# Optimization experiments

Hardware: AMD Instinct MI355X
Metric: run time of the kernel (lower is better)

The kernel has to match this reference:

```python
import jax, jax.numpy as jnp
import numpy as np

B, S, D, K = 4, 2048, 1024, 8

def setup_inputs() -> dict:
    key = jax.random.key(0)
    k1, k2, k3 = jax.random.split(key, 3)
    hidden_states = jax.random.normal(k1, (B, S, D), dtype=jnp.float32)
    # scaled so scores ~ O(1) and exp() does not overflow
    W_phi = jax.random.normal(k2, (D, D), dtype=jnp.float32) * 0.005
    W_psi = jax.random.normal(k3, (D, D), dtype=jnp.float32) * 0.005
    return {"hidden_states": hidden_states, "W_phi": W_phi, "W_psi": W_psi, "k": K}

def reference(hidden_states, W_phi, W_psi, k):
    b, s, d = hidden_states.shape
    k = min(k, s)
    # nn.Linear(bias=False): y = x @ W.T
    phi_h = hidden_states @ W_phi.T            # [b,s,d]
    psi_h = hidden_states @ W_psi.T            # [b,s,d]
    scores = jnp.einsum('bsd,btd->bst', phi_h, psi_h)  # [b,s,s]
    affinity = jnp.exp(scores)
    topk_values, topk_indices = jax.lax.top_k(affinity, k)   # [b,s,k]
    norm_sum = topk_values.sum(axis=-1, keepdims=True) + 1e-8
    normalized_weights = topk_values / norm_sum
    batch_offset = (jnp.arange(b) * s)[:, None, None]        # [b,1,1]
    src_local = jnp.arange(s)[None, :, None]                 # [1,s,1]
    src_global = jnp.broadcast_to(batch_offset + src_local, (b, s, k))
    dst_global = batch_offset + topk_indices
    mask = (topk_indices != src_local).reshape(-1)           # drop self-loops
    # eager boolean compaction (data-dependent size, like the torch module)
    src_final = src_global.reshape(-1)[mask]
    dst_final = dst_global.reshape(-1)[mask]
    weights_final = normalized_weights.reshape(-1)[mask]
    if src_final.size == 0:
        all_nodes = jnp.arange(b * s)
        return jnp.stack([all_nodes, all_nodes], axis=0), jnp.ones(b * s, dtype=jnp.float32)
    edge_index = jnp.stack([src_final, dst_final], axis=0)
    return edge_index, weights_final
```

## Files before the change

kernel.cpp:

```cpp
#include <hip/hip_runtime.h>
#include <cmath>

#define SEQ 2048
#define DDIM 1024
#define NROWS 8192
#define KSEL 8
#define NCAND 12
#define IMAXC 0x7fffffff

typedef __attribute__((ext_vector_type(8))) short bf16x8;
typedef __attribute__((ext_vector_type(4))) float f32x4;
typedef __attribute__((ext_vector_type(4))) double f64x4;

__device__ __forceinline__ unsigned short f2bf(float f) {
  unsigned u = __builtin_bit_cast(unsigned, f);
  u = (u + 0x7fffu + ((u >> 16) & 1u)) >> 16;
  return (unsigned short)u;
}
__device__ __forceinline__ float bf2f(unsigned short h) {
  unsigned u = ((unsigned)h) << 16;
  return __builtin_bit_cast(float, u);
}
__device__ __forceinline__ unsigned pkbf(float a, float b) {
  unsigned r;
  asm("v_cvt_pk_bf16_f32 %0, %1, %2" : "=v"(r) : "v"(a), "v"(b));
  return r;
}
__device__ __forceinline__ void dmap(int sel, int lg, int lr, int rg,
                                     int& ri, int& ci) {
  switch (sel) {
    case 0:  ri = (lg << 2) + rg; ci = lr; break;
    case 1:  ri = lg + (rg << 2); ci = lr; break;
    case 2:  ri = lr; ci = (lg << 2) + rg; break;
    default: ri = lr; ci = lg + (rg << 2); break;
  }
}

__global__ void kprobe(int* __restrict__ sel) {
  const int lane = threadIdx.x;
  const int lr = lane & 15, lg = lane >> 4;
  const double a = (double)(4 * lr + lg + 1);
  const double b = (double)(9 * lr + 5 * lg + 2);
  f64x4 d = (f64x4){0.0, 0.0, 0.0, 0.0};
  d = __builtin_amdgcn_mfma_f64_16x16x4f64(a, b, d, 0, 0, 0);
  int my = 4;
  for (int s = 3; s >= 0; --s) {
    bool ok = true;
    for (int rg = 0; rg < 4; ++rg) {
      int ri, ci;
      dmap(s, lg, lr, rg, ri, ci);
      double e = 0.0;
      for (int k = 0; k < 4; ++k)
        e += (double)(4 * ri + k + 1) * (double)(9 * ci + 5 * k + 2);
      ok = ok && (d[rg] == e);
    }
    if (__all(ok)) my = s;
  }
  if (lane == 0) sel[0] = my;
}

#define K0_STAGE(bi)                                        \
  do {                                                      \
    *reinterpret_cast<float4*>(&As[bi][kr][c4]) = pa0;      \
    *reinterpret_cast<float4*>(&As[bi][kr][c4 + 32]) = pa1; \
    *reinterpret_cast<float4*>(&Bs[bi][kr][c4]) = pb0;      \
    *reinterpret_cast<float4*>(&Bs[bi][kr][c4 + 32]) = pb1; \
  } while (0)

__global__ __launch_bounds__(256, 2)
void k0_mfma(const float* __restrict__ A, const float* __restrict__ B,
             float* __restrict__ C, const int* __restrict__ selp) {
  const int sel = selp[0];
  if (sel >= 4) return;
  __shared__ float As[2][32][72];
  __shared__ float Bs[2][32][72];
  const int tid = threadIdx.x;
  const int lane = tid & 63, w = tid >> 6;
  const int wr = w >> 1, wc = w & 1;
  const int lr = lane & 15, lg = lane >> 4;
  const int brow = blockIdx.y << 6, bcol = blockIdx.x << 6;
  const int kr = tid >> 3, c4 = (tid & 7) << 2;

  f64x4 acc[2][2];
#pragma unroll
  for (int mi = 0; mi < 2; ++mi)
#pragma unroll
    for (int nj = 0; nj < 2; ++nj)
      acc[mi][nj] = (f64x4){0.0, 0.0, 0.0, 0.0};

  const float* Ap = &A[(size_t)kr * DDIM + brow + c4];
  const float* Bp = &B[(size_t)kr * DDIM + bcol + c4];
  float4 pa0 = *reinterpret_cast<const float4*>(Ap);
  float4 pa1 = *reinterpret_cast<const float4*>(Ap + 32);
  float4 pb0 = *reinterpret_cast<const float4*>(Bp);
  float4 pb1 = *reinterpret_cast<const float4*>(Bp + 32);
  K0_STAGE(0);
  {
    const size_t nk = (size_t)32 * DDIM;
    pa0 = *reinterpret_cast<const float4*>(Ap + nk);
    pa1 = *reinterpret_cast<const float4*>(Ap + nk + 32);
    pb0 = *reinterpret_cast<const float4*>(Bp + nk);
    pb1 = *reinterpret_cast<const float4*>(Bp + nk + 32);
  }

  for (int t = 0; t < 32; ++t) {
    __syncthreads();
    const int cur = t & 1;
    if (t < 31) {
      K0_STAGE(cur ^ 1);
      if (t < 30) {
        const size_t nk = (size_t)(t + 2) * 32 * DDIM;
        pa0 = *reinterpret_cast<const float4*>(Ap + nk);
        pa1 = *reinterpret_cast<const float4*>(Ap + nk + 32);
        pb0 = *reinterpret_cast<const float4*>(Bp + nk);
        pb1 = *reinterpret_cast<const float4*>(Bp + nk + 32);
      }
    }
    __builtin_amdgcn_s_setprio(1);
#pragma unroll
    for (int kp = 0; kp < 8; ++kp) {
      const int ka = (kp << 2) + lg;
      double a[2], b[2];
#pragma unroll
      for (int mi = 0; mi < 2; ++mi)
        a[mi] = (double)As[cur][ka][(wr << 5) + (mi << 4) + lr];
#pragma unroll
      for (int nj = 0; nj < 2; ++nj)
        b[nj] = (double)Bs[cur][ka][(wc << 5) + (nj << 4) + lr];
#pragma unroll
      for (int mi = 0; mi < 2; ++mi)
#pragma unroll
        for (int nj = 0; nj < 2; ++nj)
          acc[mi][nj] = __builtin_amdgcn_mfma_f64_16x16x4f64(
              a[mi], b[nj], acc[mi][nj], 0, 0, 0);
    }
    __builtin_amdgcn_s_setprio(0);
  }
#pragma unroll
  for (int mi = 0; mi < 2; ++mi)
#pragma unroll
    for (int nj = 0; nj < 2; ++nj)
#pragma unroll
      for (int rg = 0; rg < 4; ++rg) {
        int ri, ci;
        dmap(sel, lg, lr, rg, ri, ci);
        C[(size_t)(brow + (wr << 5) + (mi << 4) + ri) * DDIM +
          bcol + (wc << 5) + (nj << 4) + ci] = (float)acc[mi][nj][rg];
      }
}

__global__ __launch_bounds__(256)
void k0_repair(const float* __restrict__ A, const float* __restrict__ B,
               float* __restrict__ C, const int* __restrict__ selp) {
  if (selp[0] < 4) return;
  __shared__ __align__(16) float As[32][68];
  __shared__ __align__(16) float Bs[32][68];
  const int tid = threadIdx.x;
  const int tx = tid & 15, ty = tid >> 4;
  const int brow = blockIdx.y << 6;
  const int bcol = blockIdx.x << 6;
  double acc[4][4] = {};
  for (int k0 = 0; k0 < DDIM; k0 += 32) {
#pragma unroll
    for (int i = 0; i < 2; ++i) {
      const int f = tid + (i << 8);
      const int r = f >> 4;
      const int c4 = (f & 15) << 2;
      *reinterpret_cast<float4*>(&As[r][c4]) =
          *reinterpret_cast<const float4*>(&A[(size_t)(k0 + r) * DDIM + brow + c4]);
      *reinterpret_cast<float4*>(&Bs[r][c4]) =
          *reinterpret_cast<const float4*>(&B[(size_t)(k0 + r) * DDIM + bcol + c4]);
    }
    __syncthreads();
#pragma unroll
    for (int kk = 0; kk < 32; ++kk) {
      const float4 a = *reinterpret_cast<const float4*>(&As[kk][ty << 2]);
      const float4 b = *reinterpret_cast<const float4*>(&Bs[kk][tx << 2]);
      const double ad[4] = {a.x, a.y, a.z, a.w};
      const double bd[4] = {b.x, b.y, b.z, b.w};
#pragma unroll
      for (int i = 0; i < 4; ++i)
#pragma unroll
        for (int j = 0; j < 4; ++j)
          acc[i][j] = fma(ad[i], bd[j], acc[i][j]);
    }
    __syncthreads();
  }
#pragma unroll
  for (int i = 0; i < 4; ++i) {
    float4 v = make_float4((float)acc[i][0], (float)acc[i][1],
                           (float)acc[i][2], (float)acc[i][3]);
    *reinterpret_cast<float4*>(
        &C[(size_t)(brow + (ty << 2) + i) * DDIM + bcol + (tx << 2)]) = v;
  }
}

#define K1_STAGE(bi)                                              \
  do {                                                            \
    As[bi][akh + 0][ar] = pa0.x; As[bi][akh + 1][ar] = pa0.y;     \
    As[bi][akh + 2][ar] = pa0.z; As[bi][akh + 3][ar] = pa0.w;     \
    As[bi][akh + 4][ar] = pa1.x; As[bi][akh + 5][ar] = pa1.y;     \
    As[bi][akh + 6][ar] = pa1.z; As[bi][akh + 7][ar] = pa1.w;     \
    *reinterpret_cast<float4*>(&Bs[bi][bk][bc4]) = pb0;           \
    *reinterpret_cast<float4*>(&Bs[bi][bk][bc4 + 64]) = pb1;      \
  } while (0)

__global__ __launch_bounds__(256, 2)
void k1_mfma(const float* __restrict__ A, const float* __restrict__ B,
             float* __restrict__ C, const int* __restrict__ selp) {
  const int sel = selp[0];
  if (sel >= 4) return;
  __shared__ float As[2][16][144];
  __shared__ float Bs[2][16][144];
  const int tid = threadIdx.x;
  const int lin = blockIdx.y * 8 + blockIdx.x;
  const int nlin = (lin & 7) * 64 + (lin >> 3);
  const int brow = (nlin >> 3) << 7;
  const int bcol = (nlin & 7) << 7;
  const int lane = tid & 63, w = tid >> 6;
  const int wr = w >> 1, wc = w & 1;
  const int lr = lane & 15, lg = lane >> 4;
  const int ar = tid >> 1, akh = (tid & 1) << 3;
  const int bk = tid >> 4, bc4 = (tid & 15) << 2;

  f64x4 acc[4][4];
#pragma unroll
  for (int mi = 0; mi < 4; ++mi)
#pragma unroll
    for (int nj = 0; nj < 4; ++nj)
      acc[mi][nj] = (f64x4){0.0, 0.0, 0.0, 0.0};

  const float* Ap = &A[(size_t)(brow + ar) * DDIM + akh];
  const float* Bp = &B[(size_t)bk * DDIM + bcol + bc4];

  float4 pa0 = *reinterpret_cast<const float4*>(Ap);
  float4 pa1 = *reinterpret_cast<const float4*>(Ap + 4);
  float4 pb0 = *reinterpret_cast<const float4*>(Bp);
  float4 pb1 = *reinterpret_cast<const float4*>(Bp + 64);
  K1_STAGE(0);
  pa0 = *reinterpret_cast<const float4*>(Ap + 16);
  pa1 = *reinterpret_cast<const float4*>(Ap + 20);
  pb0 = *reinterpret_cast<const float4*>(Bp + (size_t)16 * DDIM);
  pb1 = *reinterpret_cast<const float4*>(Bp + (size_t)16 * DDIM + 64);

  for (int t = 0; t < 64; ++t) {
    __syncthreads();
    const int cur = t & 1;
    if (t < 63) {
      K1_STAGE(cur ^ 1);
      if (t < 62) {
        const size_t ko = (size_t)(t + 2) << 4;
        pa0 = *reinterpret_cast<const float4*>(Ap + ko);
        pa1 = *reinterpret_cast<const float4*>(Ap + ko + 4);
        pb0 = *reinterpret_cast<const float4*>(Bp + ko * DDIM);
        pb1 = *reinterpret_cast<const float4*>(Bp + ko * DDIM + 64);
      }
    }
    __builtin_amdgcn_s_setprio(1);
#pragma unroll
    for (int kp = 0; kp < 4; ++kp) {
      const int ka = (kp << 2) + lg;
      double a[4], b[4];
#pragma unroll
      for (int mi = 0; mi < 4; ++mi)
        a[mi] = (double)As[cur][ka][(wr << 6) + (mi << 4) + lr];
#pragma unroll
      for (int nj = 0; nj < 4; ++nj)
        b[nj] = (double)Bs[cur][ka][(wc << 6) + (nj << 4) + lr];
#pragma unroll
      for (int mi = 0; mi < 4; ++mi)
#pragma unroll
        for (int nj = 0; nj < 4; ++nj)
          acc[mi][nj] = __builtin_amdgcn_mfma_f64_16x16x4f64(
              a[mi], b[nj], acc[mi][nj], 0, 0, 0);
    }
    __builtin_amdgcn_s_setprio(0);
  }
#pragma unroll
  for (int mi = 0; mi < 4; ++mi)
#pragma unroll
    for (int nj = 0; nj < 4; ++nj)
#pragma unroll
      for (int rg = 0; rg < 4; ++rg) {
        int ri, ci;
        dmap(sel, lg, lr, rg, ri, ci);
        C[(size_t)(brow + (wr << 6) + (mi << 4) + ri) * DDIM +
          bcol + (wc << 6) + (nj << 4) + ci] = (float)acc[mi][nj][rg];
      }
}

__global__ __launch_bounds__(256, 2)
void k1_repair(const float* __restrict__ A, const float* __restrict__ B,
               float* __restrict__ C, const int* __restrict__ selp) {
  if (selp[0] < 4) return;
  __shared__ double As[128][17];
  __shared__ double Bs[16][130];
  const int tid = threadIdx.x;
  const int lin = blockIdx.y * 8 + blockIdx.x;
  const int nlin = (lin & 7) * 64 + (lin >> 3);
  const int brow = (nlin >> 3) << 7;
  const int bcol = (nlin & 7) << 7;
  const int tx = tid & 15, ty = tid >> 4;
  const int ar = tid >> 1, aks = (tid & 1) << 3;
  const int bk = tid >> 4, btx = tid & 15;

  double acc[8][8];
#pragma unroll
  for (int i = 0; i < 8; ++i)
#pragma unroll
    for (int j = 0; j < 8; ++j) acc[i][j] = 0.0;

  const float* Aptr = &A[(size_t)(brow + ar) * DDIM + aks];
  const float* Bptr = &B[(size_t)bk * DDIM + bcol + (btx << 1)];

  float4 pa0, pa1;
  float2 pb[4];
  pa0 = *reinterpret_cast<const float4*>(Aptr);
  pa1 = *reinterpret_cast<const float4*>(Aptr + 4);
#pragma unroll
  for (int w = 0; w < 4; ++w)
    pb[w] = *reinterpret_cast<const float2*>(Bptr + (w << 5));

  for (int k0 = 0; k0 < DDIM; k0 += 16) {
    __syncthreads();
    As[ar][aks + 0] = (double)pa0.x; As[ar][aks + 1] = (double)pa0.y;
    As[ar][aks + 2] = (double)pa0.z; As[ar][aks + 3] = (double)pa0.w;
    As[ar][aks + 4] = (double)pa1.x; As[ar][aks + 5] = (double)pa1.y;
    As[ar][aks + 6] = (double)pa1.z; As[ar][aks + 7] = (double)pa1.w;
#pragma unroll
    for (int w = 0; w < 4; ++w) {
      Bs[bk][(btx << 1) + (w << 5) + 0] = (double)pb[w].x;
      Bs[bk][(btx << 1) + (w << 5) + 1] = (double)pb[w].y;
    }
    __syncthreads();
    if (k0 + 16 < DDIM) {
      pa0 = *reinterpret_cast<const float4*>(Aptr + k0 + 16);
      pa1 = *reinterpret_cast<const float4*>(Aptr + k0 + 20);
#pragma unroll
      for (int w = 0; w < 4; ++w)
        pb[w] = *reinterpret_cast<const float2*>(
            Bptr + (size_t)(k0 + 16) * DDIM + (w << 5));
    }
#pragma unroll 8
    for (int kk = 0; kk < 16; ++kk) {
      double a[8];
      double2 b[4];
#pragma unroll
      for (int i = 0; i < 8; ++i) a[i] = As[(ty << 3) + i][kk];
#pragma unroll
      for (int jj = 0; jj < 4; ++jj)
        b[jj] = *reinterpret_cast<const double2*>(&Bs[kk][(tx << 1) + (jj << 5)]);
#pragma unroll
      for (int i = 0; i < 8; ++i) {
#pragma unroll
        for (int jj = 0; jj < 4; ++jj) {
          acc[i][(jj << 1) + 0] = fma(a[i], b[jj].x, acc[i][(jj << 1) + 0]);
          acc[i][(jj << 1) + 1] = fma(a[i], b[jj].y, acc[i][(jj << 1) + 1]);
        }
      }
    }
  }
#pragma unroll
  for (int i = 0; i < 8; ++i) {
    float* crow = &C[(size_t)(brow + (ty << 3) + i) * DDIM + bcol + (tx << 1)];
#pragma unroll
    for (int jj = 0; jj < 4; ++jj) {
      float2 v = make_float2((float)acc[i][(jj << 1)],
                             (float)acc[i][(jj << 1) + 1]);
      *reinterpret_cast<float2*>(crow + (jj << 5)) = v;
    }
  }
}

#define K2_LOAD(koff)                                                         \
  do {                                                                        \
    _Pragma("unroll")                                                         \
    for (int q = 0; q < 4; ++q) {                                             \
      const int c = (q << 9) + tid;                                           \
      const int row = c >> 3;                                                 \
      const int gs = (c & 7) ^ (row & 7);                                     \
      const float* sT = &T[(size_t)(row0g + row) * DDIM + (koff) + (gs << 3)];\
      rT[2 * q] = *reinterpret_cast<const float4*>(sT);                       \
      rT[2 * q + 1] = *reinterpret_cast<const float4*>(sT + 4);               \
      const float* sH = &H[(size_t)(col0g + row) * DDIM + (koff) + (gs << 3)];\
      rH[2 * q] = *reinterpret_cast<const float4*>(sH);                       \
      rH[2 * q + 1] = *reinterpret_cast<const float4*>(sH + 4);               \
    }                                                                         \
  } while (0)

#define K2_STAGE(bi)                                                          \
  do {                                                                        \
    _Pragma("unroll")                                                         \
    for (int q = 0; q < 4; ++q) {                                             \
      const int c = (q << 9) + tid;                                           \
      uint4 o;                                                                \
      o.x = pkbf(rT[2 * q].x, rT[2 * q].y);                                   \
      o.y = pkbf(rT[2 * q].z, rT[2 * q].w);                                   \
      o.z = pkbf(rT[2 * q + 1].x, rT[2 * q + 1].y);                           \
      o.w = pkbf(rT[2 * q + 1].z, rT[2 * q + 1].w);                           \
      *reinterpret_cast<uint4*>(&u.stage[bi][0][c << 3]) = o;                 \
      uint4 o2;                                                               \
      o2.x = pkbf(rH[2 * q].x, rH[2 * q].y);                                  \
      o2.y = pkbf(rH[2 * q].z, rH[2 * q].w);                                  \
      o2.z = pkbf(rH[2 * q + 1].x, rH[2 * q + 1].y);                          \
      o2.w = pkbf(rH[2 * q + 1].z, rH[2 * q + 1].w);                          \
      *reinterpret_cast<uint4*>(&u.stage[bi][1][c << 3]) = o2;                \
    }                                                                         \
  } while (0)

__global__ __launch_bounds__(512, 1)
void k2_mfma(const float* __restrict__ T, const float* __restrict__ H,
             unsigned short* __restrict__ cand_v,
             unsigned char* __restrict__ cand_i) {
  __shared__ union {
    unsigned short stage[2][2][256 * 64];
    float Sl[64][264];
    struct {
      float mv[512][8];
      unsigned char mi[512][8];
    } mg;
  } u;
  const int tid = threadIdx.x;
  const int lane = tid & 63;
  const int w = tid >> 6;
  const int wr = w >> 2, wc = w & 3;
  const int lr = lane & 15, lg = lane >> 4;
  const int z = blockIdx.z;
  const int bx = blockIdx.x;
  const int brow = blockIdx.y << 8, bcol = bx << 8;
  const int row0g = z * SEQ + brow;
  const int col0g = z * SEQ + bcol;

  f32x4 acc[8][4];
#pragma unroll
  for (int mi = 0; mi < 8; ++mi)
#pragma unroll
    for (int nj = 0; nj < 4; ++nj)
      acc[mi][nj] = (f32x4){0.f, 0.f, 0.f, 0.f};

  float4 rT[8], rH[8];
  K2_LOAD(0);
  K2_STAGE(0);
  K2_LOAD(64);

  for (int t = 0; t < 16; ++t) {
    __syncthreads();
    const int cur = t & 1;
    if (t < 15) {
      K2_STAGE(cur ^ 1);
      if (t < 14) K2_LOAD((t + 2) << 6);
    }
#pragma unroll
    for (int kh = 0; kh < 2; ++kh) {
      const int sl = (kh << 2) + lg;
      bf16x8 bfv[4];
#pragma unroll
      for (int nj = 0; nj < 4; ++nj) {
        const int rb = (wc << 6) + (nj << 4) + lr;
        bfv[nj] = *reinterpret_cast<const bf16x8*>(
            &u.stage[cur][1][(rb << 6) + ((sl ^ (rb & 7)) << 3)]);
      }
#pragma unroll
      for (int mi = 0; mi < 8; ++mi) {
        const int ra = (wr << 7) + (mi << 4) + lr;
        const bf16x8 af = *reinterpret_cast<const bf16x8*>(
            &u.stage[cur][0][(ra << 6) + ((sl ^ (ra & 7)) << 3)]);
#pragma unroll
        for (int nj = 0; nj < 4; ++nj)
          acc[mi][nj] = __builtin_amdgcn_mfma_f32_16x16x32_bf16(
              af, bfv[nj], acc[mi][nj], 0, 0, 0);
      }
    }
  }

  const int srow = tid >> 3;
  const int qd = tid & 7;
#pragma unroll
  for (int p = 0; p < 4; ++p) {
    __syncthreads();
    if (wr == (p >> 1)) {
      const int mib = (p & 1) << 2;
#pragma unroll
      for (int mi2 = 0; mi2 < 4; ++mi2)
#pragma unroll
        for (int nj = 0; nj < 4; ++nj)
#pragma unroll
          for (int rg = 0; rg < 4; ++rg)
            u.Sl[(mi2 << 4) + (lg << 2) + rg][(wc << 6) + (nj << 4) + lr] =
                acc[mib + mi2][nj][rg];
    }
    __syncthreads();
    float v[KSEL];
    int ci[KSEL];
#pragma unroll
    for (int s = 0; s < KSEL; ++s) { v[s] = -3.0e38f; ci[s] = 0; }
    const int c0 = qd << 5;
    for (int c = 0; c < 32; ++c) {
      const float x = u.Sl[srow][c0 + c];
      if (x > v[KSEL - 1]) {
        float pv = x; int pc = c0 + c;
#pragma unroll
        for (int s = 0; s < KSEL; ++s) {
          if (x > v[s]) {
            const float tv = v[s]; const int tc = ci[s];
            v[s] = pv; ci[s] = pc; pv = tv; pc = tc;
          }
        }
      }
    }
    __syncthreads();
#pragma unroll
    for (int s = 0; s < KSEL; ++s) {
      u.mg.mv[tid][s] = v[s];
      u.mg.mi[tid][s] = (unsigned char)ci[s];
    }
    __syncthreads();
    if (qd == 0) {
      float fv[KSEL];
      int fi[KSEL];
#pragma unroll
      for (int s = 0; s < KSEL; ++s) { fv[s] = -3.0e38f; fi[s] = 0; }
#pragma unroll
      for (int t2 = 0; t2 < 8; ++t2) {
#pragma unroll
        for (int s = 0; s < KSEL; ++s) {
          const float x = u.mg.mv[tid + t2][s];
          const int idx = u.mg.mi[tid + t2][s];
          if (x > fv[KSEL - 1]) {
            float pv = x; int pc = idx;
#pragma unroll
            for (int s2 = 0; s2 < KSEL; ++s2) {
              if (x > fv[s2]) {
                const float tv = fv[s2]; const int tc = fi[s2];
                fv[s2] = pv; fi[s2] = pc; pv = tv; pc = tc;
              }
            }
          }
        }
      }
      const size_t base =
          (size_t)(row0g + (p << 6) + srow) * 64 + ((size_t)bx << 3);
#pragma unroll
      for (int s = 0; s < KSEL; ++s) {
        cand_v[base + s] = f2bf(fv[s]);
        cand_i[base + s] = (unsigned char)fi[s];
      }
    }
  }
}

__global__ __launch_bounds__(256)
void kr_rescore(const float* __restrict__ T, const float* __restrict__ H,
                const unsigned short* __restrict__ cand_v,
                const unsigned char* __restrict__ cand_i,
                int* __restrict__ topi, float* __restrict__ topw,
                int* __restrict__ cnt) {
  __shared__ float smv[2][2][KSEL];
  __shared__ int smi[2][2][KSEL];
  const int tid = threadIdx.x, lane = tid & 63, w = tid >> 6;
  const int rl = w >> 1;
  const int half = w & 1;
  const int r = blockIdx.x * 2 + rl;
  const int b = r >> 11, iloc = r & (SEQ - 1);

  const size_t cbase = (size_t)r * 64;
  float v0 = bf2f(cand_v[cbase + lane]);
  int i0 = ((lane >> 3) << 8) + cand_i[cbase + lane];
  int keep = 0;
  for (int rnd = 0; rnd < NCAND; ++rnd) {
    float m = v0;
#pragma unroll
    for (int off = 32; off >= 1; off >>= 1) m = fmaxf(m, __shfl_xor(m, off));
    const unsigned long long bm = __ballot(v0 == m);
    const int owner = __ffsll(bm) - 1;
    const int oi = __shfl(i0, owner);
    if (lane == owner) v0 = -3.0e38f;
    if (lane == rnd) keep = oi;
  }

  const float* Trow = T + (size_t)r * DDIM;
  float4 t4[4];
#pragma unroll
  for (int q = 0; q < 4; ++q)
    t4[q] = *reinterpret_cast<const float4*>(&Trow[(q << 8) + (lane << 2)]);

  float t8v[KSEL];
  int t8i[KSEL];
#pragma unroll
  for (int p = 0; p < KSEL; ++p) { t8v[p] = -1.0f; t8i[p] = IMAXC; }

  const int c0 = half * (NCAND / 2);
  for (int c = c0; c < c0 + NCAND / 2; ++c) {
    const int j = __shfl(keep, c);
    const float* Hrow = H + ((size_t)(b << 11) + j) * DDIM;
    double s = 0.0;
#pragma unroll
    for (int q = 0; q < 4; ++q) {
      const float4 h = *reinterpret_cast<const float4*>(&Hrow[(q << 8) + (lane << 2)]);
      s = fma((double)t4[q].x, (double)h.x, s);
      s = fma((double)t4[q].y, (double)h.y, s);
      s = fma((double)t4[q].z, (double)h.z, s);
      s = fma((double)t4[q].w, (double)h.w, s);
    }
#pragma unroll
    for (int off = 1; off < 64; off <<= 1) s += __shfl_xor(s, off);
    const float aff = expf((float)s);
    const bool g7 = (aff > t8v[KSEL - 1]) ||
                    (aff == t8v[KSEL - 1] && j < t8i[KSEL - 1]);
    if (g7) {
      float pv = aff; int pi = j;
#pragma unroll
      for (int p = 0; p < KSEL; ++p) {
        const bool g = (aff > t8v[p]) || (aff == t8v[p] && j < t8i[p]);
        if (g) {
          const float tv = t8v[p]; const int ti = t8i[p];
          t8v[p] = pv; t8i[p] = pi; pv = tv; pi = ti;
        }
      }
    }
  }

  if (lane == 0) {
#pragma unroll
    for (int p = 0; p < KSEL; ++p) {
      smv[rl][half][p] = t8v[p];
      smi[rl][half][p] = t8i[p];
    }
  }
  __syncthreads();
  if (half == 0 && lane == 0) {
#pragma unroll
    for (int p = 0; p < KSEL; ++p) {
      const float x = smv[rl][1][p];
      const int jx = smi[rl][1][p];
      const bool g7 = (x > t8v[KSEL - 1]) ||
                      (x == t8v[KSEL - 1] && jx < t8i[KSEL - 1]);
      if (g7) {
        float pv = x; int pi = jx;
#pragma unroll
        for (int q = 0; q < KSEL; ++q) {
          const bool g = (x > t8v[q]) || (x == t8v[q] && jx < t8i[q]);
          if (g) {
            const float tv = t8v[q]; const int ti = t8i[q];
            t8v[q] = pv; t8i[q] = pi; pv = tv; pi = ti;
          }
        }
      }
    }
    float sum = 0.0f;
#pragma unroll
    for (int p = 0; p < KSEL; ++p) sum += t8v[p];
    sum += 1e-8f;
    int c8 = KSEL;
#pragma unroll
    for (int p = 0; p < KSEL; ++p)
      if (t8i[p] == iloc) --c8;
    cnt[r] = c8;
#pragma unroll
    for (int p = 0; p < KSEL; ++p) {
      topi[(size_t)r * KSEL + p] = t8i[p];
      topw[(size_t)r * KSEL + p] = t8v[p] / sum;
    }
  }
}

__global__ __launch_bounds__(1024)
void k4_scan(const int* __restrict__ cnt, int* __restrict__ off) {
  __shared__ int part[1024];
  const int t = threadIdx.x;
  int loc[8];
  int s = 0;
#pragma unroll
  for (int i = 0; i < 8; ++i) { loc[i] = s; s += cnt[t * 8 + i]; }
  part[t] = s;
  __syncthreads();
  for (int d = 1; d < 1024; d <<= 1) {
    const int add = (t >= d) ? part[t - d] : 0;
    __syncthreads();
    part[t] += add;
    __syncthreads();
  }
  const int base = (t == 0) ? 0 : part[t - 1];
#pragma unroll
  for (int i = 0; i < 8; ++i) off[t * 8 + i] = base + loc[i];
}

__global__ __launch_bounds__(256)
void k5_emit(const int* __restrict__ topi, const float* __restrict__ topw,
             const int* __restrict__ off, float* __restrict__ out, int E) {
  const int r = blockIdx.x * 256 + threadIdx.x;
  if (r >= NROWS) return;
  const int o = off[r];
  const int sloc = r & (SEQ - 1);
  const int bbase = r & ~(SEQ - 1);
  int e = 0;
#pragma unroll
  for (int p = 0; p < KSEL; ++p) {
    const int id = topi[(size_t)r * KSEL + p];
    const float w = topw[(size_t)r * KSEL + p];
    if (id != sloc) {
      const int pos = o + e;
      if (pos < E) {
        out[pos] = (float)r;
        out[(size_t)E + pos] = (float)(bbase + id);
        out[2 * (size_t)E + pos] = w;
      }
      ++e;
    }
  }
}

extern "C" void kernel_launch(void* const* d_in, const int* in_sizes, int n_in,
                              void* d_out, int out_size, void* d_ws,
                              size_t ws_size, hipStream_t stream) {
  const float* H = (const float*)d_in[0];
  const float* Wphi = (const float*)d_in[1];
  const float* Wpsi = (const float*)d_in[2];
  float* out = (float*)d_out;
  const int E = out_size / 3;

  char* base = (char*)d_ws;
  float* T = (float*)base;
  char* regionX = base + 33554432;
  float* Wc = (float*)regionX;
  unsigned short* cand_v = (unsigned short*)regionX;
  unsigned char* cand_i = (unsigned char*)(regionX + 2097152);
  char* pp = regionX + 4194304;
  int* topi = (int*)pp;  pp += 262144;
  float* topw = (float*)pp; pp += 262144;
  int* cnt = (int*)pp;   pp += 32768;
  int* off = (int*)pp;   pp += 32768;
  int* sel = (int*)pp;

  kprobe<<<dim3(1), 64, 0, stream>>>(sel);
  k0_mfma<<<dim3(16, 16), 256, 0, stream>>>(Wphi, Wpsi, Wc, sel);
  k0_repair<<<dim3(16, 16), 256, 0, stream>>>(Wphi, Wpsi, Wc, sel);
  k1_mfma<<<dim3(8, 64), 256, 0, stream>>>(H, Wc, T, sel);
  k1_repair<<<dim3(8, 64), 256, 0, stream>>>(H, Wc, T, sel);
  k2_mfma<<<dim3(8, 8, 4), 512, 0, stream>>>(T, H, cand_v, cand_i);
  kr_rescore<<<dim3(NROWS / 2), 256, 0, stream>>>(T, H, cand_v, cand_i,
                                                  topi, topw, cnt);
  k4_scan<<<dim3(1), 1024, 0, stream>>>(cnt, off);
  k5_emit<<<dim3(NROWS / 256), 256, 0, stream>>>(topi, topw, off, out, E);
}
```

Measured before the change: 557.2 us.

## Pre-convert T and H to bf16 buffers so the score GEMM loads half the bytes

The projection kernels now also write a bf16 copy of T, and a new kernel converts the hidden states to bf16. A new score kernel reads these bf16 buffers directly instead of loading fp32 and converting while staging. The aim is to halve the global traffic and drop the conversion work inside the main candidate GEMM. In exchange there are extra writes in k1, an extra conversion pass over H, and more workspace. The fast path runs only when the workspace is large enough.

```diff
diff --git a/kernel.cpp b/kernel.cpp
--- a/kernel.cpp
+++ b/kernel.cpp
@@ -207,7 +207,8 @@
 
 __global__ __launch_bounds__(256, 2)
 void k1_mfma(const float* __restrict__ A, const float* __restrict__ B,
-             float* __restrict__ C, const int* __restrict__ selp) {
+             float* __restrict__ C, unsigned short* __restrict__ Tb,
+             const int* __restrict__ selp) {
   const int sel = selp[0];
   if (sel >= 4) return;
   __shared__ float As[2][16][144];
@@ -276,6 +277,7 @@
     }
     __builtin_amdgcn_s_setprio(0);
   }
+  const bool wtb = (Tb != nullptr);
 #pragma unroll
   for (int mi = 0; mi < 4; ++mi)
 #pragma unroll
@@ -284,14 +286,18 @@
       for (int rg = 0; rg < 4; ++rg) {
         int ri, ci;
         dmap(sel, lg, lr, rg, ri, ci);
-        C[(size_t)(brow + (wr << 6) + (mi << 4) + ri) * DDIM +
-          bcol + (wc << 6) + (nj << 4) + ci] = (float)acc[mi][nj][rg];
+        const size_t idx = (size_t)(brow + (wr << 6) + (mi << 4) + ri) * DDIM +
+                           bcol + (wc << 6) + (nj << 4) + ci;
+        const float v = (float)acc[mi][nj][rg];
+        C[idx] = v;
+        if (wtb) Tb[idx] = f2bf(v);
       }
 }
 
 __global__ __launch_bounds__(256, 2)
 void k1_repair(const float* __restrict__ A, const float* __restrict__ B,
-               float* __restrict__ C, const int* __restrict__ selp) {
+               float* __restrict__ C, unsigned short* __restrict__ Tb,
+               const int* __restrict__ selp) {
   if (selp[0] < 4) return;
   __shared__ double As[128][17];
   __shared__ double Bs[16][130];
@@ -360,14 +366,196 @@
       }
     }
   }
+  const bool wtb = (Tb != nullptr);
 #pragma unroll
   for (int i = 0; i < 8; ++i) {
-    float* crow = &C[(size_t)(brow + (ty << 3) + i) * DDIM + bcol + (tx << 1)];
+    const size_t rowi = (size_t)(brow + (ty << 3) + i);
+    float* crow = &C[rowi * DDIM + bcol + (tx << 1)];
 #pragma unroll
     for (int jj = 0; jj < 4; ++jj) {
       float2 v = make_float2((float)acc[i][(jj << 1)],
                              (float)acc[i][(jj << 1) + 1]);
       *reinterpret_cast<float2*>(crow + (jj << 5)) = v;
+      if (wtb)
+        *reinterpret_cast<unsigned*>(
+            &Tb[rowi * DDIM + bcol + (tx << 1) + (jj << 5)]) = pkbf(v.x, v.y);
+    }
+  }
+}
+
+__global__ __launch_bounds__(256)
+void kh(const float* __restrict__ Hin, unsigned short* __restrict__ Hb) {
+  const size_t i = ((size_t)blockIdx.x * 256 + threadIdx.x) << 3;
+  const float4 a0 = *reinterpret_cast<const float4*>(&Hin[i]);
+  const float4 a1 = *reinterpret_cast<const float4*>(&Hin[i + 4]);
+  uint4 o;
+  o.x = pkbf(a0.x, a0.y); o.y = pkbf(a0.z, a0.w);
+  o.z = pkbf(a1.x, a1.y); o.w = pkbf(a1.z, a1.w);
+  *reinterpret_cast<uint4*>(&Hb[i]) = o;
+}
+
+#define K2B_LOAD(koff)                                                        \
+  do {                                                                        \
+    _Pragma("unroll")                                                         \
+    for (int q = 0; q < 4; ++q) {                                             \
+      const int c = (q << 9) + tid;                                           \
+      const int row = c >> 3;                                                 \
+      const int gs = (c & 7) ^ (row & 7);                                     \
+      rT[q] = *reinterpret_cast<const uint4*>(                                \
+          &Tb[(size_t)(row0g + row) * DDIM + (koff) + (gs << 3)]);            \
+      rH[q] = *reinterpret_cast<const uint4*>(                                \
+          &Hb[(size_t)(col0g + row) * DDIM + (koff) + (gs << 3)]);            \
+    }                                                                         \
+  } while (0)
+
+#define K2B_STAGE(bi)                                                         \
+  do {                                                                        \
+    _Pragma("unroll")                                                         \
+    for (int q = 0; q < 4; ++q) {                                             \
+      const int c = (q << 9) + tid;                                           \
+      *reinterpret_cast<uint4*>(&u.stage[bi][0][c << 3]) = rT[q];             \
+      *reinterpret_cast<uint4*>(&u.stage[bi][1][c << 3]) = rH[q];             \
+    }                                                                         \
+  } while (0)
+
+__global__ __launch_bounds__(512, 1)
+void k2_mfma_b(const unsigned short* __restrict__ Tb,
+               const unsigned short* __restrict__ Hb,
+               unsigned short* __restrict__ cand_v,
+               unsigned char* __restrict__ cand_i) {
+  __shared__ union {
+    unsigned short stage[2][2][256 * 64];
+    float Sl[64][264];
+    struct {
+      float mv[512][8];
+      unsigned char mi[512][8];
+    } mg;
+  } u;
+  const int tid = threadIdx.x;
+  const int lane = tid & 63;
+  const int w = tid >> 6;
+  const int wr = w >> 2, wc = w & 3;
+  const int lr = lane & 15, lg = lane >> 4;
+  const int z = blockIdx.z;
+  const int bx = blockIdx.x;
+  const int brow = blockIdx.y << 8, bcol = bx << 8;
+  const int row0g = z * SEQ + brow;
+  const int col0g = z * SEQ + bcol;
+
+  f32x4 acc[8][4];
+#pragma unroll
+  for (int mi = 0; mi < 8; ++mi)
+#pragma unroll
+    for (int nj = 0; nj < 4; ++nj)
+      acc[mi][nj] = (f32x4){0.f, 0.f, 0.f, 0.f};
+
+  uint4 rT[4], rH[4];
+  K2B_LOAD(0);
+  K2B_STAGE(0);
+  K2B_LOAD(64);
+
+  for (int t = 0; t < 16; ++t) {
+    __syncthreads();
+    const int cur = t & 1;
+    if (t < 15) {
+      K2B_STAGE(cur ^ 1);
+      if (t < 14) K2B_LOAD((t + 2) << 6);
+    }
+#pragma unroll
+    for (int kh2 = 0; kh2 < 2; ++kh2) {
+      const int sl = (kh2 << 2) + lg;
+      bf16x8 bfv[4];
+#pragma unroll
+      for (int nj = 0; nj < 4; ++nj) {
+        const int rb = (wc << 6) + (nj << 4) + lr;
+        bfv[nj] = *reinterpret_cast<const bf16x8*>(
+            &u.stage[cur][1][(rb << 6) + ((sl ^ (rb & 7)) << 3)]);
+      }
+#pragma unroll
+      for (int mi = 0; mi < 8; ++mi) {
+        const int ra = (wr << 7) + (mi << 4) + lr;
+        const bf16x8 af = *reinterpret_cast<const bf16x8*>(
+            &u.stage[cur][0][(ra << 6) + ((sl ^ (ra & 7)) << 3)]);
+#pragma unroll
+        for (int nj = 0; nj < 4; ++nj)
+          acc[mi][nj] = __builtin_amdgcn_mfma_f32_16x16x32_bf16(
+              af, bfv[nj], acc[mi][nj], 0, 0, 0);
+      }
+    }
+  }
+
+  const int srow = tid >> 3;
+  const int qd = tid & 7;
+#pragma unroll
+  for (int p = 0; p < 4; ++p) {
+    __syncthreads();
+    if (wr == (p >> 1)) {
+      const int mib = (p & 1) << 2;
+#pragma unroll
+      for (int mi2 = 0; mi2 < 4; ++mi2)
+#pragma unroll
+        for (int nj = 0; nj < 4; ++nj)
+#pragma unroll
+          for (int rg = 0; rg < 4; ++rg)
+            u.Sl[(mi2 << 4) + (lg << 2) + rg][(wc << 6) + (nj << 4) + lr] =
+                acc[mib + mi2][nj][rg];
+    }
+    __syncthreads();
+    float v[KSEL];
+    int ci[KSEL];
+#pragma unroll
+    for (int s = 0; s < KSEL; ++s) { v[s] = -3.0e38f; ci[s] = 0; }
+    const int c0 = qd << 5;
+    for (int c = 0; c < 32; ++c) {
+      const float x = u.Sl[srow][c0 + c];
+      if (x > v[KSEL - 1]) {
+        float pv = x; int pc = c0 + c;
+#pragma unroll
+        for (int s = 0; s < KSEL; ++s) {
+          if (x > v[s]) {
+            const float tv = v[s]; const int tc = ci[s];
+            v[s] = pv; ci[s] = pc; pv = tv; pc = tc;
+          }
+        }
+      }
+    }
+    __syncthreads();
+#pragma unroll
+    for (int s = 0; s < KSEL; ++s) {
+      u.mg.mv[tid][s] = v[s];
+      u.mg.mi[tid][s] = (unsigned char)ci[s];
+    }
+    __syncthreads();
+    if (qd == 0) {
+      float fv[KSEL];
+      int fi[KSEL];
+#pragma unroll
+      for (int s = 0; s < KSEL; ++s) { fv[s] = -3.0e38f; fi[s] = 0; }
+#pragma unroll
+      for (int t2 = 0; t2 < 8; ++t2) {
+#pragma unroll
+        for (int s = 0; s < KSEL; ++s) {
+          const float x = u.mg.mv[tid + t2][s];
+          const int idx = u.mg.mi[tid + t2][s];
+          if (x > fv[KSEL - 1]) {
+            float pv = x; int pc = idx;
+#pragma unroll
+            for (int s2 = 0; s2 < KSEL; ++s2) {
+              if (x > fv[s2]) {
+                const float tv = fv[s2]; const int tc = fi[s2];
+                fv[s2] = pv; fi[s2] = pc; pv = tv; pc = tc;
+              }
+            }
+          }
+        }
+      }
+      const size_t base =
+          (size_t)(row0g + (p << 6) + srow) * 64 + ((size_t)bx << 3);
+#pragma unroll
+      for (int s = 0; s < KSEL; ++s) {
+        cand_v[base + s] = f2bf(fv[s]);
+        cand_i[base + s] = (unsigned char)fi[s];
+      }
     }
   }
 }
@@ -451,8 +639,8 @@
       if (t < 14) K2_LOAD((t + 2) << 6);
     }
 #pragma unroll
-    for (int kh = 0; kh < 2; ++kh) {
-      const int sl = (kh << 2) + lg;
+    for (int kh2 = 0; kh2 < 2; ++kh2) {
+      const int sl = (kh2 << 2) + lg;
       bf16x8 bfv[4];
 #pragma unroll
       for (int nj = 0; nj < 4; ++nj) {
@@ -732,12 +920,25 @@
   int* off = (int*)pp;   pp += 32768;
   int* sel = (int*)pp;
 
+  const size_t NEED_FAST = 72351744;
+  const bool fast = (ws_size >= NEED_FAST);
+  unsigned short* Tb = (unsigned short*)(base + 38797312);
+  unsigned short* Hb = (unsigned short*)(base + 55574528);
+
   kprobe<<<dim3(1), 64, 0, stream>>>(sel);
   k0_mfma<<<dim3(16, 16), 256, 0, stream>>>(Wphi, Wpsi, Wc, sel);
   k0_repair<<<dim3(16, 16), 256, 0, stream>>>(Wphi, Wpsi, Wc, sel);
-  k1_mfma<<<dim3(8, 64), 256, 0, stream>>>(H, Wc, T, sel);
-  k1_repair<<<dim3(8, 64), 256, 0, stream>>>(H, Wc, T, sel);
-  k2_mfma<<<dim3(8, 8, 4), 512, 0, stream>>>(T, H, cand_v, cand_i);
+
+  if (fast) {
+    k1_mfma<<<dim3(8, 64), 256, 0, stream>>>(H, Wc, T, Tb, sel);
+    k1_repair<<<dim3(8, 64), 256, 0, stream>>>(H, Wc, T, Tb, sel);
+    kh<<<dim3(4096), 256, 0, stream>>>(H, Hb);
+    k2_mfma_b<<<dim3(8, 8, 4), 512, 0, stream>>>(Tb, Hb, cand_v, cand_i);
+  } else {
+    k1_mfma<<<dim3(8, 64), 256, 0, stream>>>(H, Wc, T, nullptr, sel);
+    k1_repair<<<dim3(8, 64), 256, 0, stream>>>(H, Wc, T, nullptr, sel);
+    k2_mfma<<<dim3(8, 8, 4), 512, 0, stream>>>(T, H, cand_v, cand_i);
+  }
   kr_rescore<<<dim3(NROWS / 2), 256, 0, stream>>>(T, H, cand_v, cand_i,
                                                   topi, topw, cnt);
   k4_scan<<<dim3(1), 1024, 0, stream>>>(cnt, off);
```

Result: slower. 579.0 us (+3.9%).
